# Kernel optimization log

Hardware: AMD Instinct MI355X
Metric: run time of the kernel (lower is better)

The kernel has to match this reference:

```python
import jax, jax.numpy as jnp
import numpy as np

B, S, D, NL = 512, 200, 128, 2
N_ITEMS = 50001
DH = 2 * D
DFF = 4 * D


def layer_norm(x, g, b, eps=1e-5):
    mu = x.mean(-1, keepdims=True)
    v = ((x - mu) ** 2).mean(-1, keepdims=True)
    return (x - mu) / jnp.sqrt(v + eps) * g + b


def lru_scan(h, lamb0, mask):
    # h: (B, L, DH) complex64, lamb0: (DH,) complex64, mask: (B, L) bool
    Bb, L, Dh = h.shape
    log2_L = int(np.ceil(np.log2(L)))
    lamb = lamb0.reshape(1, Dh)
    for i in range(1, log2_L + 1):
        l = 2 ** i
        h = h.reshape(Bb * L // l, l, Dh)
        m = mask.reshape(Bb * L // l, l)
        h1, h2 = h[:, : l // 2], h[:, l // 2:]
        if i > 1:
            lamb = jnp.concatenate([lamb, lamb * lamb[-1]], axis=0)  # powers lambda^1..lambda^(l/2)
        carry_gate = m[:, l // 2 - 1 : l // 2, None].astype(h.dtype)
        h2 = h2 + lamb * h1[:, -1:] * carry_gate
        h = jnp.concatenate([h1, h2], axis=1)
    return h.reshape(Bb, L, Dh)


def _forward(token_emb, emb_ln_g, emb_ln_b, params_log,
             in_wr, in_wi, in_br, in_bi, out_wr, out_wi, out_br, out_bi,
             lru_ln_g, lru_ln_b, w1, b1, w2, b2, ffn_ln_g, ffn_ln_b,
             item_seq, item_seq_len):
    mask = item_seq > 0                      # (B, S)
    x = token_emb[item_seq]                  # (B, S, D)
    x = layer_norm(x, emb_ln_g, emb_ln_b)
    seq_len = item_seq.shape[1]
    L = 2 ** int(np.ceil(np.log2(seq_len)))
    pad = L - seq_len
    x = jnp.pad(x, ((0, 0), (pad, 0), (0, 0)))        # left-pad seq to power of 2
    m = jnp.pad(mask, ((0, 0), (pad, 0)))
    n_layers = params_log.shape[0]
    for li in range(n_layers):
        pl = jnp.exp(params_log[li])                  # (3, DH): nu, theta, gamma
        nu, theta, gamma = pl[0], pl[1], pl[2]
        lamb0 = jnp.exp(jax.lax.complex(-nu, theta))  # (DH,)
        in_w = jax.lax.complex(in_wr[li], in_wi[li])
        in_b = jax.lax.complex(in_br[li], in_bi[li])
        h = (jnp.einsum('bld,hd->blh', x.astype(jnp.complex64), in_w) + in_b) * gamma
        h = lru_scan(h, lamb0, m)
        out_w = jax.lax.complex(out_wr[li], out_wi[li])
        out_b = jax.lax.complex(out_br[li], out_bi[li])
        y = (jnp.einsum('blh,dh->bld', h, out_w) + out_b).real + x
        x = layer_norm(y, lru_ln_g[li], lru_ln_b[li])
        # positionwise FFN with residual + post-LN
        hff = jax.nn.gelu(jnp.einsum('bld,fd->blf', x, w1[li]) + b1[li], approximate=False)
        x = layer_norm(jnp.einsum('blf,df->bld', hff, w2[li]) + b2[li] + x,
                       ffn_ln_g[li], ffn_ln_b[li])
    x = x[:, -seq_len:]                               # (B, S, D)
    idx = item_seq_len - 1
    return x[jnp.arange(x.shape[0]), idx]             # (B, D)


def setup_inputs() -> dict:
    key = jax.random.key(0)
    ks = jax.random.split(key, 24)
    std = 0.02
    item_seq = jax.random.randint(ks[0], (B, S), 0, N_ITEMS)
    item_seq_len = jax.random.randint(ks[1], (B,), 1, S + 1)
    # LRU diagonal init (matches torch init)
    r_min, r_max = 0.8, 0.99
    u1 = jax.random.uniform(ks[2], (NL, DH))
    u2 = jax.random.uniform(ks[3], (NL, DH))
    nu_log = jnp.log(-0.5 * jnp.log(u1 * (r_max ** 2 - r_min ** 2) + r_min ** 2))
    theta_log = jnp.log(u2 * 2.0 * np.pi)
    gamma_log = 0.5 * jnp.log(1.0 - jnp.exp(-2.0 * jnp.exp(nu_log)))
    params_log = jnp.stack([nu_log, theta_log, gamma_log], axis=1)  # (NL, 3, DH)
    rn = lambda k, sh: jax.random.normal(k, sh, dtype=jnp.float32) * std
    return {
        'token_emb': rn(ks[4], (N_ITEMS, D)),
        'emb_ln_g': jnp.ones((D,), jnp.float32), 'emb_ln_b': jnp.zeros((D,), jnp.float32),
        'params_log': params_log,
        'in_wr': rn(ks[5], (NL, DH, D)), 'in_wi': rn(ks[6], (NL, DH, D)),
        'in_br': rn(ks[7], (NL, DH)), 'in_bi': rn(ks[8], (NL, DH)),
        'out_wr': rn(ks[9], (NL, D, DH)), 'out_wi': rn(ks[10], (NL, D, DH)),
        'out_br': rn(ks[11], (NL, D)), 'out_bi': rn(ks[12], (NL, D)),
        'lru_ln_g': jnp.ones((NL, D), jnp.float32), 'lru_ln_b': jnp.zeros((NL, D), jnp.float32),
        'w1': rn(ks[13], (NL, DFF, D)), 'b1': rn(ks[14], (NL, DFF)),
        'w2': rn(ks[15], (NL, D, DFF)), 'b2': rn(ks[16], (NL, D)),
        'ffn_ln_g': jnp.ones((NL, D), jnp.float32), 'ffn_ln_b': jnp.zeros((NL, D), jnp.float32),
        'item_seq': item_seq, 'item_seq_len': item_seq_len,
    }


def reference(token_emb, emb_ln_g, emb_ln_b, params_log,
              in_wr, in_wi, in_br, in_bi, out_wr, out_wi, out_br, out_bi,
              lru_ln_g, lru_ln_b, w1, b1, w2, b2, ffn_ln_g, ffn_ln_b,
              item_seq, item_seq_len):
    return _forward(token_emb, emb_ln_g, emb_ln_b, params_log,
                    in_wr, in_wi, in_br, in_bi, out_wr, out_wi, out_br, out_bi,
                    lru_ln_g, lru_ln_b, w1, b1, w2, b2, ffn_ln_g, ffn_ln_b,
                    item_seq, item_seq_len)
```

## Files before the change

### kernel.cpp

```cpp
#include <hip/hip_runtime.h>
#include <hip/hip_bf16.h>
#include <math.h>

#define B_TOT 512
#define SEQ   200
#define D     128
#define DH    256
#define DFF   512
#define LPAD  256
#define PADL  56
#define NLAY  2
#define SST   18

typedef __attribute__((ext_vector_type(8))) short bf16x8;
typedef __attribute__((ext_vector_type(4))) float floatx4;

static __device__ inline float bf2f(ushort u) {
    union { unsigned int i; float f; } v; v.i = ((unsigned int)u) << 16; return v.f;
}
static __device__ inline ushort f2bf(float x) {
    union { float f; unsigned int i; } v; v.f = x;
    unsigned int r = (v.i + 0x7FFFu + ((v.i >> 16) & 1u)) >> 16;
    return (ushort)r;
}
static __device__ inline unsigned int pkbf(float a, float b) {
    union { __hip_bfloat162 h; unsigned int u; } v;
    v.h = __float22bfloat162_rn(make_float2(a, b));
    return v.u;
}
static __device__ inline void gld_lds16(const void* g, void* l) {
    __builtin_amdgcn_global_load_lds(
        (const __attribute__((address_space(1))) unsigned int*)g,
        (__attribute__((address_space(3))) unsigned int*)l, 16, 0, 0);
}

static __device__ inline size_t haddr(int b, int s, int k) {
    int p  = k >> 8;
    int ch = k & 255;
    int g  = ch >> 5;
    int cl = ch & 31;
    return (((((size_t)b * 8 + g) * 2 + p) * SEQ + s) * 32 + cl);
}

__global__ void setup_all_kernel(const float* __restrict__ params_log,
                                 const float* __restrict__ in_br,
                                 const float* __restrict__ in_bi,
                                 const float* __restrict__ in_wr,
                                 const float* __restrict__ in_wi,
                                 const float* __restrict__ out_wr,
                                 const float* __restrict__ out_wi,
                                 const float* __restrict__ w1,
                                 const float* __restrict__ w2,
                                 ushort* __restrict__ Winb,
                                 ushort* __restrict__ W2effb,
                                 ushort* __restrict__ w1b,
                                 ushort* __restrict__ w2b,
                                 float* __restrict__ lam_pow,
                                 float* __restrict__ scale_in,
                                 float* __restrict__ bias_in)
{
    int idx = blockIdx.x * blockDim.x + threadIdx.x;
    int li = idx >> 16;
    int e  = idx & 65535;

    {
        int gp = e >> 12, rem = e & 4095;
        int q = rem >> 3, e8 = rem & 7;
        int r = q >> 4, cs = q & 15;
        int c16 = cs ^ (r & 7);
        int n = (r < 16) ? (gp * 16 + r) : (256 + gp * 16 + (r - 16));
        int d = c16 * 8 + e8;
        float wv = (n < DH) ? in_wr[((size_t)li * DH + n) * D + d]
                            : in_wi[((size_t)li * DH + (n - DH)) * D + d];
        Winb[idx] = f2bf(wv);
    }
    {
        int k0c = e >> 13, rem = e & 8191;
        int q = rem >> 3, e8 = rem & 7;
        int r = q >> 3, cs = q & 7;
        int c16 = cs ^ (r & 7);
        int k = k0c * 64 + c16 * 8 + e8;
        float w2v = (k < DH) ? out_wr[((size_t)li * D + r) * DH + k]
                             : -out_wi[((size_t)li * D + r) * DH + (k - DH)];
        W2effb[idx] = f2bf(w2v);
    }
    {
        int row = e >> 7, col = e & 127;
        int ffc = row >> 7, rl = row & 127;
        int c16 = col >> 3, e8 = col & 7;
        int cs = c16 ^ (rl & 7);
        w1b[li * 65536 + ffc * 16384 + rl * 128 + cs * 8 + e8] = f2bf(w1[idx]);
    }
    {
        int dd2 = e >> 9, kk = e & 511;
        int ffc = kk >> 7, klc = kk & 127;
        int c16 = klc >> 3, e8 = klc & 7;
        int cs = c16 ^ (dd2 & 7);
        w2b[li * 65536 + ffc * 16384 + dd2 * 128 + cs * 8 + e8] = f2bf(w2[idx]);
    }

    if (blockIdx.x < NLAY) {
        int pli = blockIdx.x;
        int c = threadIdx.x;
        const float* pl = params_log + (size_t)pli * 3 * DH;
        float nu = expf(pl[c]);
        float th = expf(pl[DH + c]);
        float ga = expf(pl[2 * DH + c]);
        float mag = expf(-nu);
        float lr = mag * cosf(th);
        float lim = mag * sinf(th);
        float2* lp = (float2*)(lam_pow + (size_t)pli * 65536) + (size_t)c * 128;
        float pr = lr, pi = lim;
        lp[0] = make_float2(pr, pi);
        for (int k = 1; k < 128; ++k) {
            float nr = pr * lr - pi * lim;
            float ni = pr * lim + pi * lr;
            pr = nr; pi = ni;
            lp[k] = make_float2(pr, pi);
        }
        scale_in[pli * 2 * DH + c]      = ga;
        scale_in[pli * 2 * DH + DH + c] = ga;
        bias_in[pli * 2 * DH + c]       = in_br[pli * DH + c] * ga;
        bias_in[pli * 2 * DH + DH + c]  = in_bi[pli * DH + c] * ga;
    }
}

__global__ __launch_bounds__(512) void build_rowmap_kernel(
    const int* __restrict__ lenp, int Bc,
    int* __restrict__ total, int* __restrict__ rowmap)
{
    __shared__ int pre[513];
    int tid = threadIdx.x;
    int lv = (tid < Bc) ? lenp[tid] : 0;
    pre[tid + 1] = lv;
    if (tid == 0) pre[0] = 0;
    __syncthreads();
    for (int ofs = 1; ofs < 512; ofs <<= 1) {
        int v = pre[tid + 1];
        int vv = (tid + 1 > ofs) ? pre[tid + 1 - ofs] : 0;
        __syncthreads();
        pre[tid + 1] = v + vv;
        __syncthreads();
    }
    if (tid == 0) total[0] = pre[Bc];
    if (tid < Bc) {
        int base = pre[tid];
        int n = lv;
        int rb = tid * SEQ;
        for (int s = 0; s < n; ++s) rowmap[base + s] = rb + s;
    }
}

__global__ __launch_bounds__(256) void embed_ln_kernel(
    const float* __restrict__ emb, const int* __restrict__ seq,
    const int* __restrict__ lenp,
    const float* __restrict__ g, const float* __restrict__ bt,
    ushort* __restrict__ x)
{
    int row  = blockIdx.x * 4 + (threadIdx.x >> 6);
    int lane = threadIdx.x & 63;
    int b = row / SEQ, s = row - b * SEQ;
    if (s >= lenp[b]) return;
    int item = seq[row];
    float2 v = *(const float2*)(emb + (size_t)item * D + lane * 2);
    float ssum = v.x + v.y;
#pragma unroll
    for (int o = 32; o > 0; o >>= 1) ssum += __shfl_xor(ssum, o);
    float mu = ssum * (1.0f / D);
    float d0 = v.x - mu, d1 = v.y - mu;
    float vs = d0 * d0 + d1 * d1;
#pragma unroll
    for (int o = 32; o > 0; o >>= 1) vs += __shfl_xor(vs, o);
    float rstd = rsqrtf(vs * (1.0f / D) + 1e-5f);
    float2 gg = *(const float2*)(g + lane * 2);
    float2 bb = *(const float2*)(bt + lane * 2);
    unsigned int o2 = pkbf(d0 * rstd * gg.x + bb.x, d1 * rstd * gg.y + bb.y);
    *(unsigned int*)(x + (size_t)row * D + lane * 2) = o2;
}

template <bool LAST>
__global__ __launch_bounds__(512) void inproj_scan_kernel(
    const ushort* __restrict__ X, const ushort* __restrict__ Win,
    ushort* __restrict__ H, const float2* __restrict__ lamT,
    const int* __restrict__ seq, const int* __restrict__ lenp,
    const float* __restrict__ scale_in, const float* __restrict__ bias_in)
{
    __shared__ __align__(16) char smem[36864];
    __shared__ float mkf[LPAD];
    char*  Wsm = smem;
    char*  xs  = smem + 8192;
    float* stR = (float*)smem;
    float* stI = stR + LPAD * SST;
    float2* bc   = (float2*)(smem + 16640);

    int gp = blockIdx.x, b = blockIdx.y;
    int tid = threadIdx.x;
    int l = tid & 63, w = tid >> 6;
    int ct = w & 1;
    int rq = w >> 1;
    int lr = l & 15, lq = l >> 4;
    int wbase = tid & ~63;

    int c  = tid & 15;
    int tl = tid >> 4;
    int t0 = tl * 8;

    int s_b = lenp[b] - 1;
    int tile_max = s_b >> 4;
    int nrows = (tile_max + 1) * 16;
    int tb = s_b + PADL;
    bool activeT = (t0 <= tb);

    const ushort* xrow = X + (size_t)b * SEQ * 128;
    gld_lds16(Win + (size_t)gp * 4096 + (size_t)tid * 8,
              Wsm + (size_t)wbase * 16);
    int nrA = nrows < 112 ? nrows : 112;
#pragma unroll
    for (int it = 0; it < 4; ++it) {
        int rbase = it * 32 + w * 4;
        int r = rbase + lq;
        int cs = lr ^ (r & 7);
        if (r < nrA)
            gld_lds16(xrow + (size_t)r * 128 + cs * 8, xs + rbase * 256);
    }

    const float2* myl = lamT + (size_t)(gp * 16 + c) * 128;

    if (tid < LPAD) {
        int t = tid;
        float m = 0.f;
        if (t >= PADL) m = (seq[(size_t)b * SEQ + (t - PADL)] > 0) ? 1.f : 0.f;
        mkf[t] = m;
    }
    __syncthreads();

    bf16x8 wf[4];
#pragma unroll
    for (int kk = 0; kk < 4; ++kk) {
        int ca = kk * 4 + lq;
        int wr = ct * 16 + lr;
        wf[kk] = *(const bf16x8*)(Wsm + wr * 256 + ((ca ^ (wr & 7)) * 16));
    }
    int tstart = rq ? (3 * rq + 1) : 0;
    int tcnt   = rq ? 3 : 4;
    floatx4 acc[4];
#pragma unroll
    for (int tt = 0; tt < 4; ++tt) acc[tt] = (floatx4)0.f;

    if (rq < 2) {
#pragma unroll
        for (int tt = 0; tt < 4; ++tt) {
            if (tt < tcnt && (tstart + tt) <= tile_max) {
                int t  = tstart + tt;
                int ar = t * 16 + lr;
#pragma unroll
                for (int kk = 0; kk < 4; ++kk) {
                    int ca = kk * 4 + lq;
                    bf16x8 af = *(const bf16x8*)(xs + ar * 256 + ((ca ^ (ar & 7)) * 16));
                    acc[tt] = __builtin_amdgcn_mfma_f32_16x16x32_bf16(wf[kk], af, acc[tt], 0, 0, 0);
                }
            }
        }
    }
    __syncthreads();

    if (nrows > 112) {
        int nrB = nrows < 200 ? nrows : 200;
#pragma unroll
        for (int it = 0; it < 3; ++it) {
            int rbase = it * 32 + w * 4;
            int rl_ = rbase + lq;
            int gr = 112 + rl_;
            int cs = lr ^ (rl_ & 7);
            if (gr < nrB)
                gld_lds16(xrow + (size_t)gr * 128 + cs * 8, xs + rbase * 256);
        }
    }
    __syncthreads();

    if (rq >= 2) {
#pragma unroll
        for (int tt = 0; tt < 4; ++tt) {
            if (tt < tcnt && (tstart + tt) <= tile_max) {
                int t  = tstart + tt;
                int ar = (t - 7) * 16 + lr;
#pragma unroll
                for (int kk = 0; kk < 4; ++kk) {
                    int ca = kk * 4 + lq;
                    bf16x8 af = *(const bf16x8*)(xs + ar * 256 + ((ca ^ (ar & 7)) * 16));
                    acc[tt] = __builtin_amdgcn_mfma_f32_16x16x32_bf16(wf[kk], af, acc[tt], 0, 0, 0);
                }
            }
        }
    }
    __syncthreads();

    float2 l14[4];
#pragma unroll
    for (int k = 0; k < 4; ++k) l14[k] = myl[k];
    float2 myl9 = myl[8];
    float2 lam_e[3];
#pragma unroll
    for (int i = 0; i < 3; ++i) {
        int half = 32 << i;
        int off = t0 & ((half << 1) - 1);
        int e = off - half;
        lam_e[i] = myl[e < 0 ? 0 : e];
    }
    float2 l7;
    l7.x = l14[3].x * l14[2].x - l14[3].y * l14[2].y;
    l7.y = l14[3].x * l14[2].y + l14[3].y * l14[2].x;

    for (int idx = tid; idx < PADL * SST; idx += 512) { stR[idx] = 0.f; stI[idx] = 0.f; }
    {
        float4 g4 = *(const float4*)(scale_in + ct * 256 + gp * 16 + lq * 4);
        float4 b4 = *(const float4*)(bias_in  + ct * 256 + gp * 16 + lq * 4);
        float* dst = ct ? stI : stR;
#pragma unroll
        for (int tt = 0; tt < 4; ++tt) {
            if (tt < tcnt && (tstart + tt) <= tile_max) {
                int t = tstart + tt;
                int s = t * 16 + lr;
                if (s <= s_b) {
                    int pos = s + PADL;
                    dst[pos * SST + lq * 4 + 0] = acc[tt][0] * g4.x + b4.x;
                    dst[pos * SST + lq * 4 + 1] = acc[tt][1] * g4.y + b4.y;
                    dst[pos * SST + lq * 4 + 2] = acc[tt][2] * g4.z + b4.z;
                    dst[pos * SST + lq * 4 + 3] = acc[tt][3] * g4.w + b4.w;
                }
            }
        }
    }
    __syncthreads();

    float xr[8], xi[8];
    if (activeT) {
#pragma unroll
        for (int k = 0; k < 8; ++k) {
            xr[k] = stR[(t0 + k) * SST + c];
            xi[k] = stI[(t0 + k) * SST + c];
        }
        float mf[8];
#pragma unroll
        for (int k = 0; k < 8; ++k) mf[k] = mkf[t0 + k];

#pragma unroll
        for (int k = 0; k < 8; k += 2) {
            float sr = xr[k] * mf[k], si = xi[k] * mf[k];
            xr[k+1] += l14[0].x * sr - l14[0].y * si;
            xi[k+1] += l14[0].x * si + l14[0].y * sr;
        }
#pragma unroll
        for (int k = 1; k < 8; k += 4) {
            float sr = xr[k] * mf[k], si = xi[k] * mf[k];
            xr[k+1] += l14[0].x * sr - l14[0].y * si;
            xi[k+1] += l14[0].x * si + l14[0].y * sr;
            xr[k+2] += l14[1].x * sr - l14[1].y * si;
            xi[k+2] += l14[1].x * si + l14[1].y * sr;
        }
        {
            float sr = xr[3] * mf[3], si = xi[3] * mf[3];
#pragma unroll
            for (int j = 0; j < 4; ++j) {
                xr[4+j] += l14[j].x * sr - l14[j].y * si;
                xi[4+j] += l14[j].x * si + l14[j].y * sr;
            }
        }
    } else {
        xr[7] = 0.f; xi[7] = 0.f;
    }

    float Ctr = 0.f, Cti = 0.f;

    {
        float svx = __shfl_xor(xr[7], 16);
        float svy = __shfl_xor(xi[7], 16);
        if (activeT && (tl & 1)) {
            float m = mkf[t0 - 1];
            float sr = svx * m, si = svy * m;
            float cr = l14[0].x * sr - l14[0].y * si;
            float ci = l14[0].x * si + l14[0].y * sr;
            Ctr += cr; Cti += ci;
            xr[7] += l7.x * cr - l7.y * ci;
            xi[7] += l7.x * ci + l7.y * cr;
        }
    }
    {
        float svx = __shfl(xr[7], 16 + c);
        float svy = __shfl(xi[7], 16 + c);
        if (activeT && (tl & 2)) {
            float m = mkf[(t0 & ~31) + 15];
            float2 le = (tl & 1) ? myl9 : l14[0];
            float sr = svx * m, si = svy * m;
            float cr = le.x * sr - le.y * si;
            float ci = le.x * si + le.y * sr;
            Ctr += cr; Cti += ci;
            xr[7] += l7.x * cr - l7.y * ci;
            xi[7] += l7.x * ci + l7.y * cr;
        }
    }
    __syncthreads();

#pragma unroll
    for (int i = 6; i <= 8; ++i) {
        int half = 1 << (i - 1);
        if (half > tb) continue;
        int buf = (i & 1) * 544;
        if (activeT) bc[buf + tl * 17 + c] = make_float2(xr[7], xi[7]);
        __syncthreads();
        int off = t0 & ((half << 1) - 1);
        if (activeT && off >= half) {
            int srcp = t0 - off + half - 1;
            float m = mkf[srcp];
            float2 sv = bc[buf + (srcp >> 3) * 17 + c];
            float2 le = lam_e[i - 6];
            float sr = sv.x * m, si = sv.y * m;
            float cr = le.x * sr - le.y * si;
            float ci = le.x * si + le.y * sr;
            Ctr += cr; Cti += ci;
            xr[7] += l7.x * cr - l7.y * ci;
            xi[7] += l7.x * ci + l7.y * cr;
        }
    }
    __syncthreads();

    if (activeT && (!LAST || (unsigned)(tb - t0) < 7u)) {
        float2 l5, l6;
        l5.x = l14[3].x * l14[0].x - l14[3].y * l14[0].y;
        l5.y = l14[3].x * l14[0].y + l14[3].y * l14[0].x;
        l6.x = l14[3].x * l14[1].x - l14[3].y * l14[1].y;
        l6.y = l14[3].x * l14[1].y + l14[3].y * l14[1].x;
        xr[0] += Ctr;                               xi[0] += Cti;
        xr[1] += l14[0].x*Ctr - l14[0].y*Cti;       xi[1] += l14[0].x*Cti + l14[0].y*Ctr;
        xr[2] += l14[1].x*Ctr - l14[1].y*Cti;       xi[2] += l14[1].x*Cti + l14[1].y*Ctr;
        xr[3] += l14[2].x*Ctr - l14[2].y*Cti;       xi[3] += l14[2].x*Cti + l14[2].y*Ctr;
        xr[4] += l14[3].x*Ctr - l14[3].y*Cti;       xi[4] += l14[3].x*Cti + l14[3].y*Ctr;
        xr[5] += l5.x*Ctr - l5.y*Cti;               xi[5] += l5.x*Cti + l5.y*Ctr;
        xr[6] += l6.x*Ctr - l6.y*Cti;               xi[6] += l6.x*Cti + l6.y*Ctr;
    }

    if (LAST) {
        if (activeT && (unsigned)(tb - t0) < 8u) {
#pragma unroll
            for (int k = 0; k < 8; ++k)
                if (t0 + k == tb) {
                    stR[tb * SST + c] = xr[k];
                    stI[tb * SST + c] = xi[k];
                }
        }
    } else {
        if (activeT && tl >= 7) {
#pragma unroll
            for (int k = 0; k < 8; ++k) {
                stR[(t0 + k) * SST + c] = xr[k];
                stI[(t0 + k) * SST + c] = xi[k];
            }
        }
    }
    __syncthreads();

    if (LAST) {
        if (tid < 32) {
            int t = tb;
            int p = tid >> 4, cc = tid & 15;
            float v = (p ? stI : stR)[t * SST + cc];
            H[(size_t)b * 512 + p * 256 + gp * 16 + cc] = f2bf(v);
        }
    } else {
        int g  = gp >> 1;
        int hc = (gp & 1) * 16;
        ushort* baseg = H + (size_t)(b * 8 + g) * 2 * SEQ * 32 + hc;
#pragma unroll
        for (int it = 0; it < 4; ++it) {
            int idx4 = it * 512 + tid;
            if (idx4 < 2 * SEQ * 4) {
                int q  = idx4 & 3;
                int ps = idx4 >> 2;
                int p  = ps >= SEQ;
                int s  = ps - p * SEQ;
                if (s > s_b) continue;
                int t  = s + PADL;
                const float* sp = (p ? stI : stR) + t * SST + q * 4;
                float2 a = *(const float2*)(sp);
                float2 d = *(const float2*)(sp + 2);
                uint2 raw;
                raw.x = pkbf(a.x, a.y);
                raw.y = pkbf(d.x, d.y);
                *(uint2*)(baseg + (size_t)ps * 32 + q * 4) = raw;
            }
        }
    }
}

__global__ __launch_bounds__(512) void outproj_kernel(
    const ushort* __restrict__ A, const ushort* __restrict__ Wimg,
    ushort* __restrict__ Cout,
    const int* __restrict__ rowmap, const int* __restrict__ totalp,
    const float* __restrict__ e0,
    const ushort* __restrict__ res,
    const float* __restrict__ lng, const float* __restrict__ lnb)
{
    int m0 = blockIdx.x * 256;
    int total = totalp[0];
    if (m0 >= total) return;
    __shared__ __align__(16) char As[32768];
    __shared__ __align__(16) char Bs[16384];
    __shared__ float2 lnS[2][256];
    int tid = threadIdx.x;
    int l = tid & 63, w = tid >> 6;
    int chh = w >> 2;
    int rh  = w & 3;
    int lr = l & 15, lq = l >> 4;
    int wbase = tid & ~63;

    int cst = tid & 7;
    int rr  = tid >> 3;
    int sb[4], ss[4];
#pragma unroll
    for (int it = 0; it < 4; ++it) {
        int gr = m0 + it * 64 + rr;
        if (gr >= total) gr = total - 1;
        int rm = rowmap[gr];
        sb[it] = rm / SEQ; ss[it] = rm - sb[it] * SEQ;
    }

    floatx4 acc[4][4];
#pragma unroll
    for (int i = 0; i < 4; ++i)
#pragma unroll
        for (int j = 0; j < 4; ++j) acc[i][j] = (floatx4)0.f;

    for (int k0c = 0; k0c < 8; ++k0c) {
        int k0 = k0c * 64;
        {
            const ushort* img = Wimg + (size_t)k0c * 8192;
#pragma unroll
            for (int it = 0; it < 2; ++it)
                gld_lds16(img + (size_t)(it * 512 + tid) * 8,
                          Bs + (size_t)(it * 512 + wbase) * 16);
        }
#pragma unroll
        for (int it = 0; it < 4; ++it) {
            int r = it * 64 + rr;
            uint4 va = *(const uint4*)(A + haddr(sb[it], ss[it], k0 + cst * 8));
            *(uint4*)(As + r * 128 + ((cst ^ (r & 7)) * 16)) = va;
        }
        __syncthreads();
#pragma unroll
        for (int kk = 0; kk < 2; ++kk) {
            bf16x8 wf[4], af[4];
            int ca = kk * 4 + lq;
#pragma unroll
            for (int i = 0; i < 4; ++i) {
                int rb = chh * 64 + i * 16 + lr;
                wf[i] = *(const bf16x8*)(Bs + rb * 128 + ((ca ^ (rb & 7)) * 16));
                int ra = rh * 64 + i * 16 + lr;
                af[i] = *(const bf16x8*)(As + ra * 128 + ((ca ^ (ra & 7)) * 16));
            }
#pragma unroll
            for (int i = 0; i < 4; ++i)
#pragma unroll
                for (int j = 0; j < 4; ++j)
                    acc[i][j] = __builtin_amdgcn_mfma_f32_16x16x32_bf16(
                        wf[i], af[j], acc[i][j], 0, 0, 0);
        }
        __syncthreads();
    }

    int chb[4], arow[4], rmj[4];
#pragma unroll
    for (int i = 0; i < 4; ++i) chb[i] = chh * 64 + i * 16 + lq * 4;
#pragma unroll
    for (int j = 0; j < 4; ++j) {
        arow[j] = m0 + rh * 64 + j * 16 + lr;
        int rc = arow[j] < total ? arow[j] : total - 1;
        rmj[j] = rowmap[rc];
    }

    {
        float4 bias[4], gv[4], bv[4];
#pragma unroll
        for (int i = 0; i < 4; ++i) {
            bias[i] = *(const float4*)(e0 + chb[i]);
            gv[i]   = *(const float4*)(lng + chb[i]);
            bv[i]   = *(const float4*)(lnb + chb[i]);
        }
#pragma unroll
        for (int j = 0; j < 4; ++j) {
#pragma unroll
            for (int i = 0; i < 4; ++i) {
                ushort4 r4 = *(const ushort4*)(res + (size_t)rmj[j] * 128 + chb[i]);
                acc[i][j][0] += ((const float*)&bias[i])[0] + bf2f(r4.x);
                acc[i][j][1] += ((const float*)&bias[i])[1] + bf2f(r4.y);
                acc[i][j][2] += ((const float*)&bias[i])[2] + bf2f(r4.z);
                acc[i][j][3] += ((const float*)&bias[i])[3] + bf2f(r4.w);
            }
        }
#pragma unroll
        for (int j = 0; j < 4; ++j) {
            float s = 0.f, q = 0.f;
#pragma unroll
            for (int i = 0; i < 4; ++i)
#pragma unroll
                for (int reg = 0; reg < 4; ++reg) {
                    float v = acc[i][j][reg];
                    s += v; q += v * v;
                }
            s += __shfl_xor(s, 16); q += __shfl_xor(q, 16);
            s += __shfl_xor(s, 32); q += __shfl_xor(q, 32);
            if (lq == 0) lnS[chh][rh * 64 + j * 16 + lr] = make_float2(s, q);
        }
        __syncthreads();
#pragma unroll
        for (int j = 0; j < 4; ++j) {
            int rl = rh * 64 + j * 16 + lr;
            float2 s0 = lnS[0][rl], s1 = lnS[1][rl];
            float mu  = (s0.x + s1.x) * (1.0f / 128.0f);
            float var = (s0.y + s1.y) * (1.0f / 128.0f) - mu * mu;
            float rstd = rsqrtf(var + 1e-5f);
            if (arow[j] < total) {
#pragma unroll
                for (int i = 0; i < 4; ++i) {
                    uint2 u;
                    u.x = pkbf((acc[i][j][0] - mu) * rstd * ((const float*)&gv[i])[0] + ((const float*)&bv[i])[0],
                               (acc[i][j][1] - mu) * rstd * ((const float*)&gv[i])[1] + ((const float*)&bv[i])[1]);
                    u.y = pkbf((acc[i][j][2] - mu) * rstd * ((const float*)&gv[i])[2] + ((const float*)&bv[i])[2],
                               (acc[i][j][3] - mu) * rstd * ((const float*)&gv[i])[3] + ((const float*)&bv[i])[3]);
                    *(uint2*)(Cout + (size_t)rmj[j] * 128 + chb[i]) = u;
                }
            }
        }
    }
}

__global__ __launch_bounds__(512) void outproj_last_kernel(
    const ushort* __restrict__ Hc, const ushort* __restrict__ Wimg,
    ushort* __restrict__ xc, int Bc,
    const float* __restrict__ e0,
    const ushort* __restrict__ Xres, const int* __restrict__ lenp,
    const float* __restrict__ lng, const float* __restrict__ lnb)
{
    __shared__ __align__(16) char As[32768];
    __shared__ __align__(16) char Bs[16384];
    __shared__ float2 lnS[2][256];
    int tid = threadIdx.x;
    int l = tid & 63, w = tid >> 6;
    int chh = w >> 2;
    int rh  = w & 3;
    int lr = l & 15, lq = l >> 4;
    int m0 = blockIdx.x * 256;
    int wbase = tid & ~63;

    int cst = tid & 7;
    int rr  = tid >> 3;

    floatx4 acc[4][4];
#pragma unroll
    for (int i = 0; i < 4; ++i)
#pragma unroll
        for (int j = 0; j < 4; ++j) acc[i][j] = (floatx4)0.f;

    for (int k0c = 0; k0c < 8; ++k0c) {
        int k0 = k0c * 64;
        {
            const ushort* img = Wimg + (size_t)k0c * 8192;
#pragma unroll
            for (int it = 0; it < 2; ++it)
                gld_lds16(img + (size_t)(it * 512 + tid) * 8,
                          Bs + (size_t)(it * 512 + wbase) * 16);
        }
#pragma unroll
        for (int it = 0; it < 4; ++it) {
            int r = it * 64 + rr;
            int gr = m0 + r; if (gr >= Bc) gr = Bc - 1;
            uint4 va = *(const uint4*)(Hc + (size_t)gr * 512 + k0 + cst * 8);
            *(uint4*)(As + r * 128 + ((cst ^ (r & 7)) * 16)) = va;
        }
        __syncthreads();
#pragma unroll
        for (int kk = 0; kk < 2; ++kk) {
            bf16x8 wf[4], af[4];
            int ca = kk * 4 + lq;
#pragma unroll
            for (int i = 0; i < 4; ++i) {
                int rb = chh * 64 + i * 16 + lr;
                wf[i] = *(const bf16x8*)(Bs + rb * 128 + ((ca ^ (rb & 7)) * 16));
                int ra = rh * 64 + i * 16 + lr;
                af[i] = *(const bf16x8*)(As + ra * 128 + ((ca ^ (ra & 7)) * 16));
            }
#pragma unroll
            for (int i = 0; i < 4; ++i)
#pragma unroll
                for (int j = 0; j < 4; ++j)
                    acc[i][j] = __builtin_amdgcn_mfma_f32_16x16x32_bf16(
                        wf[i], af[j], acc[i][j], 0, 0, 0);
        }
        __syncthreads();
    }

    int chb[4], arow[4];
#pragma unroll
    for (int i = 0; i < 4; ++i) chb[i] = chh * 64 + i * 16 + lq * 4;
#pragma unroll
    for (int j = 0; j < 4; ++j) arow[j] = m0 + rh * 64 + j * 16 + lr;

    {
        float4 bias[4], gv[4], bv[4];
#pragma unroll
        for (int i = 0; i < 4; ++i) {
            bias[i] = *(const float4*)(e0 + chb[i]);
            gv[i]   = *(const float4*)(lng + chb[i]);
            bv[i]   = *(const float4*)(lnb + chb[i]);
        }
#pragma unroll
        for (int j = 0; j < 4; ++j) {
            int br = arow[j] < Bc ? arow[j] : Bc - 1;
            int sb_ = lenp[br] - 1;
            const ushort* rbase = Xres + ((size_t)br * SEQ + sb_) * 128;
#pragma unroll
            for (int i = 0; i < 4; ++i) {
                ushort4 r4 = *(const ushort4*)(rbase + chb[i]);
                acc[i][j][0] += ((const float*)&bias[i])[0] + bf2f(r4.x);
                acc[i][j][1] += ((const float*)&bias[i])[1] + bf2f(r4.y);
                acc[i][j][2] += ((const float*)&bias[i])[2] + bf2f(r4.z);
                acc[i][j][3] += ((const float*)&bias[i])[3] + bf2f(r4.w);
            }
        }
#pragma unroll
        for (int j = 0; j < 4; ++j) {
            float s = 0.f, q = 0.f;
#pragma unroll
            for (int i = 0; i < 4; ++i)
#pragma unroll
                for (int reg = 0; reg < 4; ++reg) {
                    float v = acc[i][j][reg];
                    s += v; q += v * v;
                }
            s += __shfl_xor(s, 16); q += __shfl_xor(q, 16);
            s += __shfl_xor(s, 32); q += __shfl_xor(q, 32);
            if (lq == 0) lnS[chh][rh * 64 + j * 16 + lr] = make_float2(s, q);
        }
        __syncthreads();
#pragma unroll
        for (int j = 0; j < 4; ++j) {
            int rl = rh * 64 + j * 16 + lr;
            float2 s0 = lnS[0][rl], s1 = lnS[1][rl];
            float mu  = (s0.x + s1.x) * (1.0f / 128.0f);
            float var = (s0.y + s1.y) * (1.0f / 128.0f) - mu * mu;
            float rstd = rsqrtf(var + 1e-5f);
            if (arow[j] < Bc) {
#pragma unroll
                for (int i = 0; i < 4; ++i) {
                    uint2 u;
                    u.x = pkbf((acc[i][j][0] - mu) * rstd * ((const float*)&gv[i])[0] + ((const float*)&bv[i])[0],
                               (acc[i][j][1] - mu) * rstd * ((const float*)&gv[i])[1] + ((const float*)&bv[i])[1]);
                    u.y = pkbf((acc[i][j][2] - mu) * rstd * ((const float*)&gv[i])[2] + ((const float*)&bv[i])[2],
                               (acc[i][j][3] - mu) * rstd * ((const float*)&gv[i])[3] + ((const float*)&bv[i])[3]);
                    *(uint2*)(xc + (size_t)arow[j] * 128 + chb[i]) = u;
                }
            }
        }
    }
}

__global__ __launch_bounds__(256) void ffn_fused_kernel(
    ushort* __restrict__ X, const ushort* __restrict__ W1,
    const ushort* __restrict__ W2,
    const float* __restrict__ b1, const float* __restrict__ b2,
    const float* __restrict__ lng, const float* __restrict__ lnb,
    int Mtot, const int* __restrict__ rowmap, const int* __restrict__ totalp)
{
    int m0 = blockIdx.x * 64;
    int total = totalp ? totalp[0] : Mtot;
    if (m0 >= total) return;
    __shared__ __align__(16) char Bs[32768];
    __shared__ ushort Ps[64 * 136];
    __shared__ float2 lnS[2][64];
    int tid = threadIdx.x;
    int l = tid & 63, w = tid >> 6;
    int chh = w >> 1, rh = w & 1;
    int lr = l & 15, lq = l >> 4;
    int wbase = tid & ~63;

    int arow[2], rmrow[2];
#pragma unroll
    for (int j = 0; j < 2; ++j) {
        arow[j] = m0 + rh * 32 + j * 16 + lr;
        int rc = arow[j] < total ? arow[j] : total - 1;
        rmrow[j] = rowmap ? rowmap[rc] : rc;
    }

    bf16x8 af_x[8];
#pragma unroll
    for (int j = 0; j < 2; ++j)
#pragma unroll
        for (int kk2 = 0; kk2 < 4; ++kk2) {
            int k = kk2 * 32 + lq * 8;
            af_x[(j << 2) | kk2] = *(const bf16x8*)(X + (size_t)rmrow[j] * 128 + k);
        }

    floatx4 acc2[4][2];
#pragma unroll
    for (int i = 0; i < 4; ++i)
#pragma unroll
        for (int j = 0; j < 2; ++j) acc2[i][j] = (floatx4)0.f;

    for (int ffc = 0; ffc < 4; ++ffc) {
        if (ffc) __syncthreads();
        {
            const ushort* img = W1 + (size_t)ffc * 16384;
#pragma unroll
            for (int it = 0; it < 8; ++it)
                gld_lds16(img + (size_t)(it * 256 + tid) * 8,
                          Bs + (size_t)(it * 256 + wbase) * 16);
        }
        __syncthreads();

        floatx4 acc1[4][2];
#pragma unroll
        for (int i = 0; i < 4; ++i)
#pragma unroll
            for (int j = 0; j < 2; ++j) acc1[i][j] = (floatx4)0.f;
#pragma unroll
        for (int kk2 = 0; kk2 < 4; ++kk2) {
            int ca = kk2 * 4 + lq;
            bf16x8 wf[4];
#pragma unroll
            for (int i = 0; i < 4; ++i) {
                int rb = chh * 64 + i * 16 + lr;
                wf[i] = *(const bf16x8*)(Bs + rb * 256 + ((ca ^ (rb & 7)) * 16));
            }
#pragma unroll
            for (int i = 0; i < 4; ++i)
#pragma unroll
                for (int j = 0; j < 2; ++j)
                    acc1[i][j] = __builtin_amdgcn_mfma_f32_16x16x32_bf16(
                        wf[i], af_x[(j << 2) | kk2], acc1[i][j], 0, 0, 0);
        }

#pragma unroll
        for (int j = 0; j < 2; ++j) {
            int rowl = rh * 32 + j * 16 + lr;
#pragma unroll
            for (int i = 0; i < 4; ++i) {
                int ch0 = chh * 64 + i * 16 + lq * 4;
                float4 bv = *(const float4*)(b1 + ffc * 128 + ch0);
                float g0, g1, g2, g3, v;
                v = acc1[i][j][0] + bv.x; g0 = 0.5f * v * (1.0f + erff(v * 0.70710678118654752f));
                v = acc1[i][j][1] + bv.y; g1 = 0.5f * v * (1.0f + erff(v * 0.70710678118654752f));
                v = acc1[i][j][2] + bv.z; g2 = 0.5f * v * (1.0f + erff(v * 0.70710678118654752f));
                v = acc1[i][j][3] + bv.w; g3 = 0.5f * v * (1.0f + erff(v * 0.70710678118654752f));
                uint2 u; u.x = pkbf(g0, g1); u.y = pkbf(g2, g3);
                *(uint2*)(Ps + rowl * 136 + ch0) = u;
            }
        }
        __syncthreads();

        {
            const ushort* img = W2 + (size_t)ffc * 16384;
#pragma unroll
            for (int it = 0; it < 8; ++it)
                gld_lds16(img + (size_t)(it * 256 + tid) * 8,
                          Bs + (size_t)(it * 256 + wbase) * 16);
        }
        __syncthreads();

#pragma unroll
        for (int kk2 = 0; kk2 < 4; ++kk2) {
            int ca = kk2 * 4 + lq;
            bf16x8 wf[4], af[2];
#pragma unroll
            for (int i = 0; i < 4; ++i) {
                int rb = chh * 64 + i * 16 + lr;
                wf[i] = *(const bf16x8*)(Bs + rb * 256 + ((ca ^ (rb & 7)) * 16));
            }
#pragma unroll
            for (int j = 0; j < 2; ++j) {
                int rowl = rh * 32 + j * 16 + lr;
                af[j] = *(const bf16x8*)(Ps + rowl * 136 + kk2 * 32 + lq * 8);
            }
#pragma unroll
            for (int i = 0; i < 4; ++i)
#pragma unroll
                for (int j = 0; j < 2; ++j)
                    acc2[i][j] = __builtin_amdgcn_mfma_f32_16x16x32_bf16(
                        wf[i], af[j], acc2[i][j], 0, 0, 0);
        }
    }

    int chb[4];
#pragma unroll
    for (int i = 0; i < 4; ++i) chb[i] = chh * 64 + i * 16 + lq * 4;

    float4 bias[4], gv[4], bv[4];
#pragma unroll
    for (int i = 0; i < 4; ++i) {
        bias[i] = *(const float4*)(b2 + chb[i]);
        gv[i]   = *(const float4*)(lng + chb[i]);
        bv[i]   = *(const float4*)(lnb + chb[i]);
    }
#pragma unroll
    for (int j = 0; j < 2; ++j) {
#pragma unroll
        for (int i = 0; i < 4; ++i) {
            ushort4 r4 = *(const ushort4*)(X + (size_t)rmrow[j] * 128 + chb[i]);
            acc2[i][j][0] += ((const float*)&bias[i])[0] + bf2f(r4.x);
            acc2[i][j][1] += ((const float*)&bias[i])[1] + bf2f(r4.y);
            acc2[i][j][2] += ((const float*)&bias[i])[2] + bf2f(r4.z);
            acc2[i][j][3] += ((const float*)&bias[i])[3] + bf2f(r4.w);
        }
    }
#pragma unroll
    for (int j = 0; j < 2; ++j) {
        float s = 0.f, q = 0.f;
#pragma unroll
        for (int i = 0; i < 4; ++i)
#pragma unroll
            for (int reg = 0; reg < 4; ++reg) {
                float v = acc2[i][j][reg];
                s += v; q += v * v;
            }
        s += __shfl_xor(s, 16); q += __shfl_xor(q, 16);
        s += __shfl_xor(s, 32); q += __shfl_xor(q, 32);
        if (lq == 0) lnS[chh][rh * 32 + j * 16 + lr] = make_float2(s, q);
    }
    __syncthreads();
#pragma unroll
    for (int j = 0; j < 2; ++j) {
        int rl = rh * 32 + j * 16 + lr;
        float2 s0 = lnS[0][rl], s1 = lnS[1][rl];
        float mu  = (s0.x + s1.x) * (1.0f / 128.0f);
        float var = (s0.y + s1.y) * (1.0f / 128.0f) - mu * mu;
        float rstd = rsqrtf(var + 1e-5f);
        if (arow[j] < total) {
#pragma unroll
            for (int i = 0; i < 4; ++i) {
                uint2 u;
                u.x = pkbf((acc2[i][j][0] - mu) * rstd * ((const float*)&gv[i])[0] + ((const float*)&bv[i])[0],
                           (acc2[i][j][1] - mu) * rstd * ((const float*)&gv[i])[1] + ((const float*)&bv[i])[1]);
                u.y = pkbf((acc2[i][j][2] - mu) * rstd * ((const float*)&gv[i])[2] + ((const float*)&bv[i])[2],
                           (acc2[i][j][3] - mu) * rstd * ((const float*)&gv[i])[3] + ((const float*)&bv[i])[3]);
                *(uint2*)(X + (size_t)rmrow[j] * 128 + chb[i]) = u;
            }
        }
    }
}

__global__ void gather_final_kernel(const ushort* __restrict__ xc,
                                    float* __restrict__ out, int b0, int Bc)
{
    int i = blockIdx.x * 256 + threadIdx.x;
    if (i >= Bc * D) return;
    out[(size_t)b0 * D + i] = bf2f(xc[i]);
}

extern "C" void kernel_launch(void* const* d_in, const int* in_sizes, int n_in,
                              void* d_out, int out_size, void* d_ws, size_t ws_size,
                              hipStream_t stream)
{
    const float* token_emb  = (const float*)d_in[0];
    const float* emb_ln_g   = (const float*)d_in[1];
    const float* emb_ln_b   = (const float*)d_in[2];
    const float* params_log = (const float*)d_in[3];
    const float* in_wr      = (const float*)d_in[4];
    const float* in_wi      = (const float*)d_in[5];
    const float* in_br      = (const float*)d_in[6];
    const float* in_bi      = (const float*)d_in[7];
    const float* out_wr     = (const float*)d_in[8];
    const float* out_wi     = (const float*)d_in[9];
    const float* out_br     = (const float*)d_in[10];
    const float* lru_ln_g   = (const float*)d_in[12];
    const float* lru_ln_b   = (const float*)d_in[13];
    const float* w1         = (const float*)d_in[14];
    const float* b1         = (const float*)d_in[15];
    const float* w2         = (const float*)d_in[16];
    const float* b2         = (const float*)d_in[17];
    const float* ffn_ln_g   = (const float*)d_in[18];
    const float* ffn_ln_b   = (const float*)d_in[19];
    const int*   item_seq   = (const int*)d_in[20];
    const int*   item_seq_len = (const int*)d_in[21];
    float* out = (float*)d_out;

    char* ws = (char*)d_ws;
    ushort* Winb   = (ushort*)ws;                      ws += NLAY * 65536 * 2;
    ushort* W2effb = (ushort*)ws;                      ws += NLAY * 65536 * 2;
    ushort* w1b    = (ushort*)ws;                      ws += NLAY * 65536 * 2;
    ushort* w2b    = (ushort*)ws;                      ws += NLAY * 65536 * 2;
    float* lam_pow = (float*)ws;                       ws += NLAY * 65536 * 4;
    float* scale_in = (float*)ws;                      ws += NLAY * 512 * 4;
    float* bias_in  = (float*)ws;                      ws += NLAY * 512 * 4;
    size_t table_bytes = (size_t)(ws - (char*)d_ws);

    int Bc = B_TOT;
    while (Bc > 32) {
        size_t need = table_bytes
                    + (size_t)Bc * SEQ * (D * 2 + 2 * DH * 2)
                    + (size_t)(Bc * SEQ + 8) * 4 + 1024;
        if (need <= ws_size) break;
        Bc >>= 1;
    }
    ushort* xb = (ushort*)ws;                          ws += (size_t)Bc * SEQ * D * 2;
    ushort* hb = (ushort*)ws;                          ws += (size_t)Bc * SEQ * 2 * DH * 2;
    int* totalp = (int*)ws;                            ws += 8 * 4;
    int* rowmap = (int*)ws;
    ushort* Hc = hb;
    ushort* xc = hb + (size_t)Bc * 512;

    setup_all_kernel<<<NLAY * 65536 / 256, 256, 0, stream>>>(
        params_log, in_br, in_bi, in_wr, in_wi, out_wr, out_wi, w1, w2,
        Winb, W2effb, w1b, w2b, lam_pow, scale_in, bias_in);

    for (int b0 = 0; b0 < B_TOT; b0 += Bc) {
        int M = Bc * SEQ;
        const int* lenp = item_seq_len + b0;
        build_rowmap_kernel<<<1, 512, 0, stream>>>(lenp, Bc, totalp, rowmap);
        embed_ln_kernel<<<M / 4, 256, 0, stream>>>(
            token_emb, item_seq + (size_t)b0 * SEQ, lenp,
            emb_ln_g, emb_ln_b, xb);

        for (int li = 0; li < NLAY; ++li) {
            if (li < NLAY - 1) {
                inproj_scan_kernel<false><<<dim3(16, Bc), 512, 0, stream>>>(
                    xb, Winb + (size_t)li * 65536, hb,
                    (const float2*)(lam_pow + (size_t)li * 65536),
                    item_seq + (size_t)b0 * SEQ, lenp,
                    scale_in + li * 512, bias_in + li * 512);
                outproj_kernel<<<dim3(M / 256), 512, 0, stream>>>(
                    hb, W2effb + (size_t)li * 65536, xb, rowmap, totalp,
                    out_br + li * D, xb,
                    lru_ln_g + li * D, lru_ln_b + li * D);
                ffn_fused_kernel<<<dim3(M / 64), 256, 0, stream>>>(
                    xb, w1b + (size_t)li * 65536, w2b + (size_t)li * 65536,
                    b1 + li * DFF, b2 + li * D,
                    ffn_ln_g + li * D, ffn_ln_b + li * D, M, rowmap, totalp);
            } else {
                inproj_scan_kernel<true><<<dim3(16, Bc), 512, 0, stream>>>(
                    xb, Winb + (size_t)li * 65536, Hc,
                    (const float2*)(lam_pow + (size_t)li * 65536),
                    item_seq + (size_t)b0 * SEQ, lenp,
                    scale_in + li * 512, bias_in + li * 512);
                outproj_last_kernel<<<dim3((Bc + 255) / 256), 512, 0, stream>>>(
                    Hc, W2effb + (size_t)li * 65536, xc, Bc,
                    out_br + li * D, xb, lenp,
                    lru_ln_g + li * D, lru_ln_b + li * D);
                ffn_fused_kernel<<<dim3((Bc + 63) / 64), 256, 0, stream>>>(
                    xc, w1b + (size_t)li * 65536, w2b + (size_t)li * 65536,
                    b1 + li * DFF, b2 + li * D,
                    ffn_ln_g + li * D, ffn_ln_b + li * D, Bc,
                    (const int*)0, (const int*)0);
            }
        }
        gather_final_kernel<<<(Bc * D + 255) / 256, 256, 0, stream>>>(
            xc, out, b0, Bc);
    }
}
```

Baseline: 444.8 us.

## Transpose scan staging to channel-major and do the whole cross-chunk tree with wave shuffles

The LDS staging buffer for the complex scan changes from time-major (stride 18) to channel-major (stride 260), and thread-to-work mapping is flipped so that the 32 time chunks of one channel sit in one half-wave. The upper scan levels, which previously went through LDS broadcast buffers with a __syncthreads per level, now run as in-wave __shfl operations, and per-thread loads and stores become 16-byte vector accesses. This is meant to remove block barriers and LDS round trips from the scan. In exchange the final global write-out now reads LDS with a stride of one channel, which may cause more bank conflicts.

Result: faster. 396.3 us (-10.9%).

```diff
diff --git a/kernel.cpp b/kernel.cpp
--- a/kernel.cpp
+++ b/kernel.cpp
@@ -10,7 +10,7 @@
 #define LPAD  256
 #define PADL  56
 #define NLAY  2
-#define SST   18
+#define CST   260
 
 typedef __attribute__((ext_vector_type(8))) short bf16x8;
 typedef __attribute__((ext_vector_type(4))) float floatx4;
@@ -186,12 +186,11 @@
     const float* __restrict__ scale_in, const float* __restrict__ bias_in)
 {
     __shared__ __align__(16) char smem[36864];
-    __shared__ float mkf[LPAD];
+    __shared__ __align__(16) float mkf[LPAD];
     char*  Wsm = smem;
     char*  xs  = smem + 8192;
     float* stR = (float*)smem;
-    float* stI = stR + LPAD * SST;
-    float2* bc   = (float2*)(smem + 16640);
+    float* stI = stR + 16 * CST;
 
     int gp = blockIdx.x, b = blockIdx.y;
     int tid = threadIdx.x;
@@ -201,9 +200,10 @@
     int lr = l & 15, lq = l >> 4;
     int wbase = tid & ~63;
 
-    int c  = tid & 15;
-    int tl = tid >> 4;
+    int c  = tid >> 5;
+    int tl = tid & 31;
     int t0 = tl * 8;
+    int lbase = l & 32;
 
     int s_b = lenp[b] - 1;
     int tile_max = s_b >> 4;
@@ -311,7 +311,13 @@
     l7.x = l14[3].x * l14[2].x - l14[3].y * l14[2].y;
     l7.y = l14[3].x * l14[2].y + l14[3].y * l14[2].x;
 
-    for (int idx = tid; idx < PADL * SST; idx += 512) { stR[idx] = 0.f; stI[idx] = 0.f; }
+    {
+        int zc = tid & 15, zk = tid >> 4;
+        stR[zc * CST + zk] = 0.f; stI[zc * CST + zk] = 0.f;
+        if (zk < PADL - 32) {
+            stR[zc * CST + zk + 32] = 0.f; stI[zc * CST + zk + 32] = 0.f;
+        }
+    }
     {
         float4 g4 = *(const float4*)(scale_in + ct * 256 + gp * 16 + lq * 4);
         float4 b4 = *(const float4*)(bias_in  + ct * 256 + gp * 16 + lq * 4);
@@ -323,27 +329,25 @@
                 int s = t * 16 + lr;
                 if (s <= s_b) {
                     int pos = s + PADL;
-                    dst[pos * SST + lq * 4 + 0] = acc[tt][0] * g4.x + b4.x;
-                    dst[pos * SST + lq * 4 + 1] = acc[tt][1] * g4.y + b4.y;
-                    dst[pos * SST + lq * 4 + 2] = acc[tt][2] * g4.z + b4.z;
-                    dst[pos * SST + lq * 4 + 3] = acc[tt][3] * g4.w + b4.w;
+                    dst[(lq * 4 + 0) * CST + pos] = acc[tt][0] * g4.x + b4.x;
+                    dst[(lq * 4 + 1) * CST + pos] = acc[tt][1] * g4.y + b4.y;
+                    dst[(lq * 4 + 2) * CST + pos] = acc[tt][2] * g4.z + b4.z;
+                    dst[(lq * 4 + 3) * CST + pos] = acc[tt][3] * g4.w + b4.w;
                 }
             }
         }
     }
     __syncthreads();
 
-    float xr[8], xi[8];
+    __align__(16) float xr[8], xi[8], mf[8];
+    *(floatx4*)&xr[0] = *(const floatx4*)(stR + c * CST + t0);
+    *(floatx4*)&xr[4] = *(const floatx4*)(stR + c * CST + t0 + 4);
+    *(floatx4*)&xi[0] = *(const floatx4*)(stI + c * CST + t0);
+    *(floatx4*)&xi[4] = *(const floatx4*)(stI + c * CST + t0 + 4);
+    *(floatx4*)&mf[0] = *(const floatx4*)(mkf + t0);
+    *(floatx4*)&mf[4] = *(const floatx4*)(mkf + t0 + 4);
+
     if (activeT) {
-#pragma unroll
-        for (int k = 0; k < 8; ++k) {
-            xr[k] = stR[(t0 + k) * SST + c];
-            xi[k] = stI[(t0 + k) * SST + c];
-        }
-        float mf[8];
-#pragma unroll
-        for (int k = 0; k < 8; ++k) mf[k] = mkf[t0 + k];
-
 #pragma unroll
         for (int k = 0; k < 8; k += 2) {
             float sr = xr[k] * mf[k], si = xi[k] * mf[k];
@@ -371,58 +375,31 @@
     }
 
     float Ctr = 0.f, Cti = 0.f;
-
-    {
-        float svx = __shfl_xor(xr[7], 16);
-        float svy = __shfl_xor(xi[7], 16);
-        if (activeT && (tl & 1)) {
-            float m = mkf[t0 - 1];
-            float sr = svx * m, si = svy * m;
-            float cr = l14[0].x * sr - l14[0].y * si;
-            float ci = l14[0].x * si + l14[0].y * sr;
-            Ctr += cr; Cti += ci;
-            xr[7] += l7.x * cr - l7.y * ci;
-            xi[7] += l7.x * ci + l7.y * cr;
-        }
-    }
-    {
-        float svx = __shfl(xr[7], 16 + c);
-        float svy = __shfl(xi[7], 16 + c);
-        if (activeT && (tl & 2)) {
-            float m = mkf[(t0 & ~31) + 15];
-            float2 le = (tl & 1) ? myl9 : l14[0];
-            float sr = svx * m, si = svy * m;
-            float cr = le.x * sr - le.y * si;
-            float ci = le.x * si + le.y * sr;
-            Ctr += cr; Cti += ci;
-            xr[7] += l7.x * cr - l7.y * ci;
-            xi[7] += l7.x * ci + l7.y * cr;
-        }
-    }
-    __syncthreads();
-
-#pragma unroll
-    for (int i = 6; i <= 8; ++i) {
-        int half = 1 << (i - 1);
-        if (half > tb) continue;
-        int buf = (i & 1) * 544;
-        if (activeT) bc[buf + tl * 17 + c] = make_float2(xr[7], xi[7]);
-        __syncthreads();
-        int off = t0 & ((half << 1) - 1);
-        if (activeT && off >= half) {
-            int srcp = t0 - off + half - 1;
-            float m = mkf[srcp];
-            float2 sv = bc[buf + (srcp >> 3) * 17 + c];
-            float2 le = lam_e[i - 6];
-            float sr = sv.x * m, si = sv.y * m;
-            float cr = le.x * sr - le.y * si;
-            float ci = le.x * si + le.y * sr;
-            Ctr += cr; Cti += ci;
-            xr[7] += l7.x * cr - l7.y * ci;
-            xi[7] += l7.x * ci + l7.y * cr;
-        }
-    }
-    __syncthreads();
+    float m7 = mf[7];
+    float pxr = xr[7] * m7, pxi = xi[7] * m7;
+
+#define TREE_LEVEL(SRC_TL, TGT, LE)                                          \
+    {                                                                        \
+        int srcl = lbase | (SRC_TL);                                         \
+        float svx = __shfl(pxr, srcl);                                       \
+        float svy = __shfl(pxi, srcl);                                       \
+        if (activeT && (TGT)) {                                              \
+            float2 le = (LE);                                                \
+            float cr = le.x * svx - le.y * svy;                              \
+            float ci = le.x * svy + le.y * svx;                              \
+            Ctr += cr; Cti += ci;                                            \
+            xr[7] += l7.x * cr - l7.y * ci;                                  \
+            xi[7] += l7.x * ci + l7.y * cr;                                  \
+            pxr = xr[7] * m7; pxi = xi[7] * m7;                              \
+        }                                                                    \
+    }
+
+    TREE_LEVEL(tl & ~1,          tl & 1,  l14[0]);
+    TREE_LEVEL((tl & ~3)  | 1,   tl & 2,  (tl & 1) ? myl9 : l14[0]);
+    TREE_LEVEL((tl & ~7)  | 3,   tl & 4,  lam_e[0]);
+    if (tb >= 64)  TREE_LEVEL((tl & ~15) | 7,  tl & 8,  lam_e[1]);
+    if (tb >= 128) TREE_LEVEL((tl & ~31) | 15, tl & 16, lam_e[2]);
+#undef TREE_LEVEL
 
     if (activeT && (!LAST || (unsigned)(tb - t0) < 7u)) {
         float2 l5, l6;
@@ -444,26 +421,24 @@
 #pragma unroll
             for (int k = 0; k < 8; ++k)
                 if (t0 + k == tb) {
-                    stR[tb * SST + c] = xr[k];
-                    stI[tb * SST + c] = xi[k];
+                    stR[c * CST + tb] = xr[k];
+                    stI[c * CST + tb] = xi[k];
                 }
         }
     } else {
         if (activeT && tl >= 7) {
-#pragma unroll
-            for (int k = 0; k < 8; ++k) {
-                stR[(t0 + k) * SST + c] = xr[k];
-                stI[(t0 + k) * SST + c] = xi[k];
-            }
+            *(floatx4*)(stR + c * CST + t0)     = *(const floatx4*)&xr[0];
+            *(floatx4*)(stR + c * CST + t0 + 4) = *(const floatx4*)&xr[4];
+            *(floatx4*)(stI + c * CST + t0)     = *(const floatx4*)&xi[0];
+            *(floatx4*)(stI + c * CST + t0 + 4) = *(const floatx4*)&xi[4];
         }
     }
     __syncthreads();
 
     if (LAST) {
         if (tid < 32) {
-            int t = tb;
             int p = tid >> 4, cc = tid & 15;
-            float v = (p ? stI : stR)[t * SST + cc];
+            float v = (p ? stI : stR)[cc * CST + tb];
             H[(size_t)b * 512 + p * 256 + gp * 16 + cc] = f2bf(v);
         }
     } else {
@@ -480,12 +455,14 @@
                 int s  = ps - p * SEQ;
                 if (s > s_b) continue;
                 int t  = s + PADL;
-                const float* sp = (p ? stI : stR) + t * SST + q * 4;
-                float2 a = *(const float2*)(sp);
-                float2 d = *(const float2*)(sp + 2);
+                const float* sp = p ? stI : stR;
+                float a0 = sp[(q * 4 + 0) * CST + t];
+                float a1 = sp[(q * 4 + 1) * CST + t];
+                float a2 = sp[(q * 4 + 2) * CST + t];
+                float a3 = sp[(q * 4 + 3) * CST + t];
                 uint2 raw;
-                raw.x = pkbf(a.x, a.y);
-                raw.y = pkbf(d.x, d.y);
+                raw.x = pkbf(a0, a1);
+                raw.y = pkbf(a2, a3);
                 *(uint2*)(baseg + (size_t)ps * 32 + q * 4) = raw;
             }
         }
```
